# Optimization experiments

Measured on AMD Instinct MI355X. Metric: run time of the kernel, lower is better.

Reference implementation:

```python
import jax, jax.numpy as jnp
import numpy as np

N_NODES = 65536
N_EDGES = 1048576
D_IN = 1024
D_HID = 64
N_CLS = 32


def gcn_conv(x, W, b, src, dst, n_nodes):
    """PyG GCNConv: linear transform, then symmetric-normalized aggregation
    with implicit self-loops (fill value 1)."""
    xw = x @ W  # [N, d_out]
    e = src.shape[0]
    # degree over destination index, including the self-loop (+1)
    deg = jax.ops.segment_sum(jnp.ones((e,), xw.dtype), dst, num_segments=n_nodes) + 1.0
    dinv_sqrt = jax.lax.rsqrt(deg)  # deg >= 1, safe
    norm = dinv_sqrt[src] * dinv_sqrt[dst]  # [E]
    agg = jax.ops.segment_sum(xw[src] * norm[:, None], dst, num_segments=n_nodes)
    # self-loop contribution: norm = deg_i^{-1}
    agg = agg + xw * (1.0 / deg)[:, None]
    return agg + b


def setup_inputs() -> dict:
    key = jax.random.key(0)
    k_x, k_e, k_w1, k_b1, k_w2, k_b2 = jax.random.split(key, 6)
    x = jax.random.normal(k_x, (N_NODES, D_IN), dtype=jnp.float32)
    edge_index = jax.random.randint(k_e, (2, N_EDGES), 0, N_NODES, dtype=jnp.int64)
    s1 = 1.0 / np.sqrt(D_IN)
    s2 = 1.0 / np.sqrt(D_HID)
    W1 = jax.random.uniform(k_w1, (D_IN, D_HID), jnp.float32, -s1, s1)
    b1 = jax.random.uniform(k_b1, (D_HID,), jnp.float32, -s1, s1)
    W2 = jax.random.uniform(k_w2, (D_HID, N_CLS), jnp.float32, -s2, s2)
    b2 = jax.random.uniform(k_b2, (N_CLS,), jnp.float32, -s2, s2)
    return {"x": x, "edge_index": edge_index, "W1": W1, "b1": b1, "W2": W2, "b2": b2}


def reference(x, edge_index, W1, b1, W2, b2):
    src, dst = edge_index[0], edge_index[1]
    n = x.shape[0]
    h = gcn_conv(x, W1, b1, src, dst, n)
    h = jax.nn.relu(h)
    # dropout is identity in eval mode
    h = gcn_conv(h, W2, b2, src, dst, n)
    return jax.nn.log_softmax(h, axis=1)
```

## Files before the change

### kernel.cpp

```cpp
#include <hip/hip_runtime.h>
#include <hip/hip_bf16.h>

#define N_NODES 65536
#define D_IN 1024
#define D_HID 64
#define N_CLS 32

typedef short short8 __attribute__((ext_vector_type(8)));
typedef float floatx4 __attribute__((ext_vector_type(4)));

__device__ __forceinline__ unsigned short f2bf(float f) {
  union { float f; unsigned u; } cv; cv.f = f;
  unsigned r = (cv.u + 0x7FFFu + ((cv.u >> 16) & 1u)) >> 16;
  return (unsigned short)r;
}
__device__ __forceinline__ unsigned pack_bf2(float x, float y) {
  return (unsigned)f2bf(x) | ((unsigned)f2bf(y) << 16);
}
__device__ __forceinline__ float2 bf2f2(unsigned v) {
  union { unsigned u; float f; } a, b;
  a.u = v << 16;
  b.u = v & 0xFFFF0000u;
  return make_float2(a.f, b.f);
}

__global__ void k_count(const int* __restrict__ dst, int* __restrict__ cnt, int e4) {
  int i = blockIdx.x * blockDim.x + threadIdx.x;
  if (i < e4) {
    int4 d = ((const int4*)dst)[i];
    atomicAdd(&cnt[d.x], 1);
    atomicAdd(&cnt[d.y], 1);
    atomicAdd(&cnt[d.z], 1);
    atomicAdd(&cnt[d.w], 1);
  }
}

__global__ void k_scan_a(const int* __restrict__ cnt, int* __restrict__ bsum) {
  __shared__ int s[256];
  int t = threadIdx.x;
  s[t] = cnt[blockIdx.x * 256 + t];
  __syncthreads();
  for (int off = 128; off > 0; off >>= 1) {
    if (t < off) s[t] += s[t + off];
    __syncthreads();
  }
  if (t == 0) bsum[blockIdx.x] = s[0];
}

__global__ void k_scanb_w1t(int* __restrict__ bsum, int* __restrict__ boff,
                            const float* __restrict__ w1, unsigned short* __restrict__ w1t) {
  if (blockIdx.x < 256) {
    int i = blockIdx.x * 256 + threadIdx.x;
    int k = i / D_HID, n = i % D_HID;
    w1t[n * D_IN + k] = f2bf(w1[i]);
    return;
  }
  __shared__ int s[256];
  int t = threadIdx.x;
  int v = bsum[t];
  s[t] = v;
  __syncthreads();
  for (int off = 1; off < 256; off <<= 1) {
    int x = (t >= off) ? s[t - off] : 0;
    __syncthreads();
    s[t] += x;
    __syncthreads();
  }
  boff[t] = s[t] - v;
}

__global__ void k_scan_c(const int* __restrict__ cnt, const int* __restrict__ boff,
                         int* __restrict__ rowptr, int* __restrict__ cursor,
                         float* __restrict__ dinv) {
  __shared__ int s[256];
  int t = threadIdx.x;
  int i = blockIdx.x * 256 + t;
  int v = cnt[i];
  s[t] = v;
  __syncthreads();
  for (int off = 1; off < 256; off <<= 1) {
    int x = (t >= off) ? s[t - off] : 0;
    __syncthreads();
    s[t] += x;
    __syncthreads();
  }
  int excl = s[t] - v + boff[blockIdx.x];
  rowptr[i] = excl;
  cursor[i] = excl;
  dinv[i] = rsqrtf((float)(v + 1));
  if (i == N_NODES - 1) rowptr[N_NODES] = excl + v;
}

__global__ void k_fill(const int* __restrict__ src, const int* __restrict__ dst,
                       int* __restrict__ cursor, int* __restrict__ csr_src, int e4) {
  int i = blockIdx.x * blockDim.x + threadIdx.x;
  if (i < e4) {
    int4 d = ((const int4*)dst)[i];
    int4 s = ((const int4*)src)[i];
    csr_src[atomicAdd(&cursor[d.x], 1)] = s.x;
    csr_src[atomicAdd(&cursor[d.y], 1)] = s.y;
    csr_src[atomicAdd(&cursor[d.z], 1)] = s.z;
    csr_src[atomicAdd(&cursor[d.w], 1)] = s.w;
  }
}

__global__ __launch_bounds__(256) void k_gemm1(const float* __restrict__ x,
    const unsigned short* __restrict__ w1t, const float* __restrict__ dinv,
    unsigned short* __restrict__ xw1s) {
  int wave = threadIdx.x >> 6;
  int lane = threadIdx.x & 63;
  int quad = lane >> 4;
  int l16 = lane & 15;
  int rowbase = blockIdx.x * 128 + wave * 32;
  const float* xr0 = x + (size_t)(rowbase + l16) * D_IN + quad * 8;
  const float* xr1 = xr0 + (size_t)16 * D_IN;
  floatx4 acc[2][4];
#pragma unroll
  for (int mt = 0; mt < 2; mt++)
#pragma unroll
    for (int nt = 0; nt < 4; nt++) acc[mt][nt] = (floatx4){0.f, 0.f, 0.f, 0.f};
  const unsigned short* bbase = w1t + quad * 8;
#pragma unroll 2
  for (int k0 = 0; k0 < D_IN; k0 += 32) {
    float4 a0 = *(const float4*)(xr0 + k0);
    float4 a1 = *(const float4*)(xr0 + k0 + 4);
    float4 a2 = *(const float4*)(xr1 + k0);
    float4 a3 = *(const float4*)(xr1 + k0 + 4);
    float av0[8] = {a0.x, a0.y, a0.z, a0.w, a1.x, a1.y, a1.z, a1.w};
    float av1[8] = {a2.x, a2.y, a2.z, a2.w, a3.x, a3.y, a3.z, a3.w};
    short8 af0, af1;
#pragma unroll
    for (int j = 0; j < 8; j++) { af0[j] = (short)f2bf(av0[j]); af1[j] = (short)f2bf(av1[j]); }
#pragma unroll
    for (int nt = 0; nt < 4; nt++) {
      short8 bf = *(const short8*)(bbase + (size_t)(nt * 16 + l16) * D_IN + k0);
      acc[0][nt] = __builtin_amdgcn_mfma_f32_16x16x32_bf16(af0, bf, acc[0][nt], 0, 0, 0);
      acc[1][nt] = __builtin_amdgcn_mfma_f32_16x16x32_bf16(af1, bf, acc[1][nt], 0, 0, 0);
    }
  }
#pragma unroll
  for (int mt = 0; mt < 2; mt++)
#pragma unroll
    for (int r = 0; r < 4; r++) {
      int row = rowbase + mt * 16 + quad * 4 + r;
      float sc = dinv[row];
#pragma unroll
      for (int nt = 0; nt < 4; nt++)
        xw1s[(size_t)row * D_HID + nt * 16 + l16] = f2bf(acc[mt][nt][r] * sc);
    }
}

__global__ __launch_bounds__(256) void k_agg1(const unsigned* __restrict__ xw1s2,
    const int* __restrict__ rowptr, const int* __restrict__ csr_src,
    const float* __restrict__ dinv, const float* __restrict__ b1,
    const float* __restrict__ w2, unsigned short* __restrict__ xw2s) {
  __shared__ float w2s[D_HID * N_CLS];
  __shared__ float2 hbuf[4][32];
  for (int i = threadIdx.x; i < D_HID * N_CLS; i += 256) w2s[i] = w2[i];
  __syncthreads();
  int wave = threadIdx.x >> 6;
  int lane = threadIdx.x & 63;
  int h = lane >> 5, l = lane & 31;
  int node = blockIdx.x * 4 + wave;
  float dd = dinv[node];
  int beg = rowptr[node], end = rowptr[node + 1];
  float2 c0 = {0.f, 0.f}, c1 = {0.f, 0.f}, c2 = {0.f, 0.f}, c3 = {0.f, 0.f};
  int e = beg + h;
  for (; e + 6 < end; e += 8) {
    int s0 = csr_src[e], s1 = csr_src[e + 2], s2 = csr_src[e + 4], s3 = csr_src[e + 6];
    float2 v0 = bf2f2(xw1s2[(size_t)s0 * 32 + l]);
    float2 v1 = bf2f2(xw1s2[(size_t)s1 * 32 + l]);
    float2 v2 = bf2f2(xw1s2[(size_t)s2 * 32 + l]);
    float2 v3 = bf2f2(xw1s2[(size_t)s3 * 32 + l]);
    c0.x += v0.x; c0.y += v0.y; c1.x += v1.x; c1.y += v1.y;
    c2.x += v2.x; c2.y += v2.y; c3.x += v3.x; c3.y += v3.y;
  }
  for (; e < end; e += 2) {
    float2 v = bf2f2(xw1s2[(size_t)csr_src[e] * 32 + l]);
    c0.x += v.x; c0.y += v.y;
  }
  float sx = (c0.x + c1.x) + (c2.x + c3.x);
  float sy = (c0.y + c1.y) + (c2.y + c3.y);
  sx += __shfl_down(sx, 32);
  sy += __shfl_down(sy, 32);
  if (lane < 32) {
    float2 self = bf2f2(xw1s2[(size_t)node * 32 + l]);
    float2 bb = ((const float2*)b1)[l];
    float vx = dd * (sx + self.x) + bb.x;
    float vy = dd * (sy + self.y) + bb.y;
    hbuf[wave][l] = make_float2(vx > 0.f ? vx : 0.f, vy > 0.f ? vy : 0.f);
  }
  __syncthreads();
  const float* hb = (const float*)hbuf[wave];
  int c = lane & 31;
  float p = 0.f;
#pragma unroll
  for (int kk = 0; kk < 32; kk++) {
    int k = h * 32 + kk;
    p += hb[k] * w2s[k * N_CLS + c];
  }
  p += __shfl_down(p, 32);
  if (lane < 32) xw2s[(size_t)node * N_CLS + c] = f2bf(p * dd);
}

__global__ __launch_bounds__(256) void k_agg2(const unsigned* __restrict__ xw2s2,
    const int* __restrict__ rowptr, const int* __restrict__ csr_src,
    const float* __restrict__ dinv, const float* __restrict__ b2,
    float* __restrict__ out) {
  int wave = threadIdx.x >> 6;
  int lane = threadIdx.x & 63;
  int q = lane >> 4, l = lane & 15;
  int node = blockIdx.x * 4 + wave;
  float dd = dinv[node];
  int beg = rowptr[node], end = rowptr[node + 1];
  float2 c0 = {0.f, 0.f}, c1 = {0.f, 0.f};
  int e = beg + q;
  for (; e + 4 < end; e += 8) {
    int s0 = csr_src[e], s1 = csr_src[e + 4];
    float2 v0 = bf2f2(xw2s2[(size_t)s0 * 16 + l]);
    float2 v1 = bf2f2(xw2s2[(size_t)s1 * 16 + l]);
    c0.x += v0.x; c0.y += v0.y; c1.x += v1.x; c1.y += v1.y;
  }
  for (; e < end; e += 4) {
    float2 v = bf2f2(xw2s2[(size_t)csr_src[e] * 16 + l]);
    c0.x += v.x; c0.y += v.y;
  }
  float sx = c0.x + c1.x;
  float sy = c0.y + c1.y;
  sx += __shfl_down(sx, 32); sy += __shfl_down(sy, 32);
  sx += __shfl_down(sx, 16); sy += __shfl_down(sy, 16);
  if (lane < 16) {
    float2 self = bf2f2(xw2s2[(size_t)node * 16 + l]);
    float2 bb = ((const float2*)b2)[l];
    float lx = dd * (sx + self.x) + bb.x;
    float ly = dd * (sy + self.y) + bb.y;
    float m = fmaxf(lx, ly);
#pragma unroll
    for (int o = 8; o > 0; o >>= 1) m = fmaxf(m, __shfl_xor(m, o));
    float s2 = __expf(lx - m) + __expf(ly - m);
#pragma unroll
    for (int o = 8; o > 0; o >>= 1) s2 += __shfl_xor(s2, o);
    float lse = m + __logf(s2);
    ((float2*)out)[(size_t)node * 16 + l] = make_float2(lx - lse, ly - lse);
  }
}

extern "C" void kernel_launch(void* const* d_in, const int* in_sizes, int n_in,
                              void* d_out, int out_size, void* d_ws, size_t ws_size,
                              hipStream_t stream) {
  (void)n_in; (void)out_size; (void)ws_size;
  const float* x  = (const float*)d_in[0];
  const int*   ei = (const int*)d_in[1];
  const float* w1 = (const float*)d_in[2];
  const float* b1 = (const float*)d_in[3];
  const float* w2 = (const float*)d_in[4];
  const float* b2 = (const float*)d_in[5];
  float* out = (float*)d_out;
  int e = in_sizes[1] / 2;
  const int* src = ei;
  const int* dst = ei + e;

  char* ws = (char*)d_ws;
  int* cnt            = (int*)(ws + 0x000000);
  int* rowptr         = (int*)(ws + 0x040000);
  int* cursor         = (int*)(ws + 0x0C0000);
  float* dinv         = (float*)(ws + 0x100000);
  int* bsum           = (int*)(ws + 0x140000);
  int* boff           = (int*)(ws + 0x141000);
  int* csr_src        = (int*)(ws + 0x180000);
  unsigned short* w1t = (unsigned short*)(ws + 0x580000);
  unsigned short* xw1s= (unsigned short*)(ws + 0x600000);
  unsigned short* xw2s= (unsigned short*)(ws + 0xE00000);

  int e4 = e / 4;
  hipMemsetAsync(cnt, 0, N_NODES * sizeof(int), stream);
  k_count   <<<(e4 + 255) / 256, 256, 0, stream>>>(dst, cnt, e4);
  k_scan_a  <<<N_NODES / 256, 256, 0, stream>>>(cnt, bsum);
  k_scanb_w1t<<<257, 256, 0, stream>>>(bsum, boff, w1, w1t);
  k_scan_c  <<<N_NODES / 256, 256, 0, stream>>>(cnt, boff, rowptr, cursor, dinv);
  k_fill    <<<(e4 + 255) / 256, 256, 0, stream>>>(src, dst, cursor, csr_src, e4);
  k_gemm1   <<<N_NODES / 128, 256, 0, stream>>>(x, w1t, dinv, xw1s);
  k_agg1    <<<N_NODES / 4, 256, 0, stream>>>((const unsigned*)xw1s, rowptr, csr_src,
                                              dinv, b1, w2, xw2s);
  k_agg2    <<<N_NODES / 4, 256, 0, stream>>>((const unsigned*)xw2s, rowptr, csr_src,
                                              dinv, b2, out);
}
```

Before: 602.6 us.

## Merge preprocessing kernels and overlap CSR fill with GEMM; deepen gather unroll

Folds the W1 transpose into the degree-count kernel and drops the separate block-offset scan, so each scan_c block reduces the preceding block sums itself. The CSR fill and the first GEMM now run in one launch as disjoint block ranges, letting the atomic scatter overlap the x@W1 work. The aggregation loops keep more independent gathers in flight (8 in agg1, 4 in agg2) to hide memory latency. The cost is some redundant prefix work per scan block and higher register pressure in the aggregation kernels.

```diff
diff --git a/kernel.cpp b/kernel.cpp
--- a/kernel.cpp
+++ b/kernel.cpp
@@ -13,9 +13,6 @@
   union { float f; unsigned u; } cv; cv.f = f;
   unsigned r = (cv.u + 0x7FFFu + ((cv.u >> 16) & 1u)) >> 16;
   return (unsigned short)r;
-}
-__device__ __forceinline__ unsigned pack_bf2(float x, float y) {
-  return (unsigned)f2bf(x) | ((unsigned)f2bf(y) << 16);
 }
 __device__ __forceinline__ float2 bf2f2(unsigned v) {
   union { unsigned u; float f; } a, b;
@@ -24,8 +21,17 @@
   return make_float2(a.f, b.f);
 }
 
-__global__ void k_count(const int* __restrict__ dst, int* __restrict__ cnt, int e4) {
-  int i = blockIdx.x * blockDim.x + threadIdx.x;
+__global__ void k_count_w1t(const int* __restrict__ dst, int* __restrict__ cnt,
+                            const float* __restrict__ w1, unsigned short* __restrict__ w1t,
+                            int e4) {
+  int b = blockIdx.x;
+  if (b >= 1024) {
+    int i = (b - 1024) * 256 + threadIdx.x;
+    int k = i / D_HID, n = i % D_HID;
+    w1t[n * D_IN + k] = f2bf(w1[i]);
+    return;
+  }
+  int i = b * 256 + threadIdx.x;
   if (i < e4) {
     int4 d = ((const int4*)dst)[i];
     atomicAdd(&cnt[d.x], 1);
@@ -47,33 +53,19 @@
   if (t == 0) bsum[blockIdx.x] = s[0];
 }
 
-__global__ void k_scanb_w1t(int* __restrict__ bsum, int* __restrict__ boff,
-                            const float* __restrict__ w1, unsigned short* __restrict__ w1t) {
-  if (blockIdx.x < 256) {
-    int i = blockIdx.x * 256 + threadIdx.x;
-    int k = i / D_HID, n = i % D_HID;
-    w1t[n * D_IN + k] = f2bf(w1[i]);
-    return;
-  }
-  __shared__ int s[256];
-  int t = threadIdx.x;
-  int v = bsum[t];
-  s[t] = v;
-  __syncthreads();
-  for (int off = 1; off < 256; off <<= 1) {
-    int x = (t >= off) ? s[t - off] : 0;
-    __syncthreads();
-    s[t] += x;
-    __syncthreads();
-  }
-  boff[t] = s[t] - v;
-}
-
-__global__ void k_scan_c(const int* __restrict__ cnt, const int* __restrict__ boff,
+__global__ void k_scan_c(const int* __restrict__ cnt, const int* __restrict__ bsum,
                          int* __restrict__ rowptr, int* __restrict__ cursor,
                          float* __restrict__ dinv) {
   __shared__ int s[256];
   int t = threadIdx.x;
+  s[t] = (t < blockIdx.x) ? bsum[t] : 0;
+  __syncthreads();
+  for (int off = 128; off > 0; off >>= 1) {
+    if (t < off) s[t] += s[t + off];
+    __syncthreads();
+  }
+  int blockoff = s[0];
+  __syncthreads();
   int i = blockIdx.x * 256 + t;
   int v = cnt[i];
   s[t] = v;
@@ -84,29 +76,30 @@
     s[t] += x;
     __syncthreads();
   }
-  int excl = s[t] - v + boff[blockIdx.x];
+  int excl = s[t] - v + blockoff;
   rowptr[i] = excl;
   cursor[i] = excl;
   dinv[i] = rsqrtf((float)(v + 1));
   if (i == N_NODES - 1) rowptr[N_NODES] = excl + v;
 }
 
-__global__ void k_fill(const int* __restrict__ src, const int* __restrict__ dst,
-                       int* __restrict__ cursor, int* __restrict__ csr_src, int e4) {
-  int i = blockIdx.x * blockDim.x + threadIdx.x;
-  if (i < e4) {
-    int4 d = ((const int4*)dst)[i];
-    int4 s = ((const int4*)src)[i];
-    csr_src[atomicAdd(&cursor[d.x], 1)] = s.x;
-    csr_src[atomicAdd(&cursor[d.y], 1)] = s.y;
-    csr_src[atomicAdd(&cursor[d.z], 1)] = s.z;
-    csr_src[atomicAdd(&cursor[d.w], 1)] = s.w;
-  }
-}
-
-__global__ __launch_bounds__(256) void k_gemm1(const float* __restrict__ x,
-    const unsigned short* __restrict__ w1t, const float* __restrict__ dinv,
-    unsigned short* __restrict__ xw1s) {
+__global__ __launch_bounds__(256) void k_fill_gemm1(
+    const int* __restrict__ src, const int* __restrict__ dst,
+    int* __restrict__ cursor, int* __restrict__ csr_src, int e4,
+    const float* __restrict__ x, const unsigned short* __restrict__ w1t,
+    const float* __restrict__ dinv, unsigned short* __restrict__ xw1s) {
+  if (blockIdx.x >= 512) {
+    int i = (blockIdx.x - 512) * 256 + threadIdx.x;
+    if (i < e4) {
+      int4 d = ((const int4*)dst)[i];
+      int4 s = ((const int4*)src)[i];
+      csr_src[atomicAdd(&cursor[d.x], 1)] = s.x;
+      csr_src[atomicAdd(&cursor[d.y], 1)] = s.y;
+      csr_src[atomicAdd(&cursor[d.z], 1)] = s.z;
+      csr_src[atomicAdd(&cursor[d.w], 1)] = s.w;
+    }
+    return;
+  }
   int wave = threadIdx.x >> 6;
   int lane = threadIdx.x & 63;
   int quad = lane >> 4;
@@ -164,23 +157,26 @@
   int node = blockIdx.x * 4 + wave;
   float dd = dinv[node];
   int beg = rowptr[node], end = rowptr[node + 1];
-  float2 c0 = {0.f, 0.f}, c1 = {0.f, 0.f}, c2 = {0.f, 0.f}, c3 = {0.f, 0.f};
+  float cx[8], cy[8];
+#pragma unroll
+  for (int j = 0; j < 8; j++) { cx[j] = 0.f; cy[j] = 0.f; }
   int e = beg + h;
-  for (; e + 6 < end; e += 8) {
-    int s0 = csr_src[e], s1 = csr_src[e + 2], s2 = csr_src[e + 4], s3 = csr_src[e + 6];
-    float2 v0 = bf2f2(xw1s2[(size_t)s0 * 32 + l]);
-    float2 v1 = bf2f2(xw1s2[(size_t)s1 * 32 + l]);
-    float2 v2 = bf2f2(xw1s2[(size_t)s2 * 32 + l]);
-    float2 v3 = bf2f2(xw1s2[(size_t)s3 * 32 + l]);
-    c0.x += v0.x; c0.y += v0.y; c1.x += v1.x; c1.y += v1.y;
-    c2.x += v2.x; c2.y += v2.y; c3.x += v3.x; c3.y += v3.y;
+  for (; e + 14 < end; e += 16) {
+    int idx[8];
+#pragma unroll
+    for (int j = 0; j < 8; j++) idx[j] = csr_src[e + 2 * j];
+#pragma unroll
+    for (int j = 0; j < 8; j++) {
+      float2 v = bf2f2(xw1s2[(size_t)idx[j] * 32 + l]);
+      cx[j] += v.x; cy[j] += v.y;
+    }
   }
   for (; e < end; e += 2) {
     float2 v = bf2f2(xw1s2[(size_t)csr_src[e] * 32 + l]);
-    c0.x += v.x; c0.y += v.y;
-  }
-  float sx = (c0.x + c1.x) + (c2.x + c3.x);
-  float sy = (c0.y + c1.y) + (c2.y + c3.y);
+    cx[0] += v.x; cy[0] += v.y;
+  }
+  float sx = ((cx[0] + cx[1]) + (cx[2] + cx[3])) + ((cx[4] + cx[5]) + (cx[6] + cx[7]));
+  float sy = ((cy[0] + cy[1]) + (cy[2] + cy[3])) + ((cy[4] + cy[5]) + (cy[6] + cy[7]));
   sx += __shfl_down(sx, 32);
   sy += __shfl_down(sy, 32);
   if (lane < 32) {
@@ -213,20 +209,26 @@
   int node = blockIdx.x * 4 + wave;
   float dd = dinv[node];
   int beg = rowptr[node], end = rowptr[node + 1];
-  float2 c0 = {0.f, 0.f}, c1 = {0.f, 0.f};
+  float cx[4], cy[4];
+#pragma unroll
+  for (int j = 0; j < 4; j++) { cx[j] = 0.f; cy[j] = 0.f; }
   int e = beg + q;
-  for (; e + 4 < end; e += 8) {
-    int s0 = csr_src[e], s1 = csr_src[e + 4];
-    float2 v0 = bf2f2(xw2s2[(size_t)s0 * 16 + l]);
-    float2 v1 = bf2f2(xw2s2[(size_t)s1 * 16 + l]);
-    c0.x += v0.x; c0.y += v0.y; c1.x += v1.x; c1.y += v1.y;
+  for (; e + 12 < end; e += 16) {
+    int idx[4];
+#pragma unroll
+    for (int j = 0; j < 4; j++) idx[j] = csr_src[e + 4 * j];
+#pragma unroll
+    for (int j = 0; j < 4; j++) {
+      float2 v = bf2f2(xw2s2[(size_t)idx[j] * 16 + l]);
+      cx[j] += v.x; cy[j] += v.y;
+    }
   }
   for (; e < end; e += 4) {
     float2 v = bf2f2(xw2s2[(size_t)csr_src[e] * 16 + l]);
-    c0.x += v.x; c0.y += v.y;
-  }
-  float sx = c0.x + c1.x;
-  float sy = c0.y + c1.y;
+    cx[0] += v.x; cy[0] += v.y;
+  }
+  float sx = (cx[0] + cx[1]) + (cx[2] + cx[3]);
+  float sy = (cy[0] + cy[1]) + (cy[2] + cy[3]);
   sx += __shfl_down(sx, 32); sy += __shfl_down(sy, 32);
   sx += __shfl_down(sx, 16); sy += __shfl_down(sy, 16);
   if (lane < 16) {
@@ -266,7 +268,6 @@
   int* cursor         = (int*)(ws + 0x0C0000);
   float* dinv         = (float*)(ws + 0x100000);
   int* bsum           = (int*)(ws + 0x140000);
-  int* boff           = (int*)(ws + 0x141000);
   int* csr_src        = (int*)(ws + 0x180000);
   unsigned short* w1t = (unsigned short*)(ws + 0x580000);
   unsigned short* xw1s= (unsigned short*)(ws + 0x600000);
@@ -274,14 +275,13 @@
 
   int e4 = e / 4;
   hipMemsetAsync(cnt, 0, N_NODES * sizeof(int), stream);
-  k_count   <<<(e4 + 255) / 256, 256, 0, stream>>>(dst, cnt, e4);
-  k_scan_a  <<<N_NODES / 256, 256, 0, stream>>>(cnt, bsum);
-  k_scanb_w1t<<<257, 256, 0, stream>>>(bsum, boff, w1, w1t);
-  k_scan_c  <<<N_NODES / 256, 256, 0, stream>>>(cnt, boff, rowptr, cursor, dinv);
-  k_fill    <<<(e4 + 255) / 256, 256, 0, stream>>>(src, dst, cursor, csr_src, e4);
-  k_gemm1   <<<N_NODES / 128, 256, 0, stream>>>(x, w1t, dinv, xw1s);
-  k_agg1    <<<N_NODES / 4, 256, 0, stream>>>((const unsigned*)xw1s, rowptr, csr_src,
-                                              dinv, b1, w2, xw2s);
-  k_agg2    <<<N_NODES / 4, 256, 0, stream>>>((const unsigned*)xw2s, rowptr, csr_src,
-                                              dinv, b2, out);
-}
+  k_count_w1t<<<1280, 256, 0, stream>>>(dst, cnt, w1, w1t, e4);
+  k_scan_a   <<<N_NODES / 256, 256, 0, stream>>>(cnt, bsum);
+  k_scan_c   <<<N_NODES / 256, 256, 0, stream>>>(cnt, bsum, rowptr, cursor, dinv);
+  k_fill_gemm1<<<1536, 256, 0, stream>>>(src, dst, cursor, csr_src, e4,
+                                         x, w1t, dinv, xw1s);
+  k_agg1     <<<N_NODES / 4, 256, 0, stream>>>((const unsigned*)xw1s, rowptr, csr_src,
+                                               dinv, b1, w2, xw2s);
+  k_agg2     <<<N_NODES / 4, 256, 0, stream>>>((const unsigned*)xw2s, rowptr, csr_src,
+                                               dinv, b2, out);
+}
```

After: 588.6 us. 1.02x faster.
